# Kernel tuning notes

Measured on AMD Instinct MI355X. Metric: run time of the kernel, lower is better.

The kernel has to match this reference:

```python
import jax, jax.numpy as jnp
import numpy as np

D, NH, NKV, HD, DFF, W, PLD = 2048, 8, 2, 256, 8192, 512, 256
EPS = 1e-6

def rmsnorm(x, w):
    # Gemma-style RMSNorm with (1 + weight) scaling
    return x * jax.lax.rsqrt(jnp.mean(x * x, axis=-1, keepdims=True) + EPS) * (1.0 + w)

def rmsnorm_nw(x):
    # v_norm: weightless RMSNorm
    return x * jax.lax.rsqrt(jnp.mean(x * x, axis=-1, keepdims=True) + EPS)

def rotate_half(x):
    x1, x2 = jnp.split(x, 2, axis=-1)
    return jnp.concatenate([-x2, x1], axis=-1)

def setup_inputs() -> dict:
    key = jax.random.key(0)
    ks = jax.random.split(key, 24)
    w = lambda k, shp, s=0.02: (jax.random.normal(k, shp, dtype=jnp.float32) * s)
    inp = {
        "hidden_states": jax.random.normal(ks[0], (1, 1, D), dtype=jnp.float32),
        "cos": jax.random.uniform(ks[1], (1, 1, HD), dtype=jnp.float32),
        "sin": jax.random.uniform(ks[2], (1, 1, HD), dtype=jnp.float32),
        "mask": jnp.zeros((1, 1, 1, W), dtype=jnp.float32),
        "kv_cache": jnp.zeros((2, NKV, W, HD), dtype=jnp.float32),
        "per_layer": jax.random.normal(ks[3], (1, 1, PLD), dtype=jnp.float32),
        "ln_in_w": w(ks[4], (D,)),
        "Wq": w(ks[5], (NH * HD, D)),
        "q_norm_w": w(ks[6], (HD,)),
        "Wk": w(ks[7], (NKV * HD, D)),
        "Wv": w(ks[8], (NKV * HD, D)),
        "k_norm_w": w(ks[9], (HD,)),
        "Wo": w(ks[10], (D, NH * HD)),
        "post_attn_ln_w": w(ks[11], (D,)),
        "pre_ffn_ln_w": w(ks[12], (D,)),
        "Wgate": w(ks[13], (DFF, D)),
        "Wup": w(ks[14], (DFF, D)),
        "Wdown": w(ks[15], (D, DFF)),
        "post_ffn_ln_w": w(ks[16], (D,)),
        "Wpl_gate": w(ks[17], (PLD, D)),
        "Wpl_proj": w(ks[18], (D, PLD)),
        "post_pl_ln_w": w(ks[19], (D,)),
        "layer_scalar": jnp.ones((1,), dtype=jnp.float32),
        "ring_pos": 37,
    }
    return inp

def reference(hidden_states, cos, sin, mask, kv_cache, per_layer,
              ln_in_w, Wq, q_norm_w, Wk, Wv, k_norm_w, Wo,
              post_attn_ln_w, pre_ffn_ln_w, Wgate, Wup, Wdown, post_ffn_ln_w,
              Wpl_gate, Wpl_proj, post_pl_ln_w, layer_scalar, ring_pos):
    n_rep = NH // NKV
    x = hidden_states[0, 0]                      # (D,)
    residual = x
    h = rmsnorm(x, ln_in_w)                      # input_layernorm
    c, s = cos[0, 0], sin[0, 0]                  # (HD,)
    # q/k/v projections (seq=1 decode -> GEMV)
    q = (h @ Wq.T).reshape(NH, HD)
    q = rmsnorm(q, q_norm_w)
    q = q * c + rotate_half(q) * s               # RoPE
    k = (h @ Wk.T).reshape(NKV, HD)
    k = rmsnorm(k, k_norm_w)
    k = k * c + rotate_half(k) * s
    v = rmsnorm_nw((h @ Wv.T).reshape(NKV, HD))
    # slice-write into the ring-buffer KV cache
    kv = kv_cache.at[0, :, ring_pos, :].set(k).at[1, :, ring_pos, :].set(v)
    K, V = kv[0], kv[1]                          # (NKV, W, HD)
    # GQA: repeat kv heads n_rep times
    Kx = jnp.repeat(K, n_rep, axis=0)            # (NH, W, HD)
    Vx = jnp.repeat(V, n_rep, axis=0)
    scores = jnp.einsum('hd,hwd->hw', q, Kx) + mask[0, 0, 0]   # no 1/sqrt(hd), as in source
    attn = jax.nn.softmax(scores, axis=-1)
    o = jnp.einsum('hw,hwd->hd', attn, Vx).reshape(NH * HD)
    attn_out = rmsnorm(o @ Wo.T, post_attn_ln_w)
    x = residual + attn_out
    # gated-GELU MLP
    residual = x
    hn = rmsnorm(x, pre_ffn_ln_w)
    gate = jax.nn.gelu(hn @ Wgate.T, approximate=True)
    mlp = ((gate * (hn @ Wup.T)) @ Wdown.T)
    x = residual + rmsnorm(mlp, post_ffn_ln_w)
    # per-layer input gate/projection
    residual = x
    g = jax.nn.gelu(x @ Wpl_gate.T, approximate=True) * per_layer[0, 0]
    g = rmsnorm(g @ Wpl_proj.T, post_pl_ln_w)
    x = (residual + g) * layer_scalar[0]
    return x.reshape(1, 1, D)

if __name__ == '__main__':
    out = reference(**setup_inputs())
    print(out.shape, out.dtype)
```

## Files before the change

kernel.cpp:

```cpp
#include <hip/hip_runtime.h>
#include <math.h>

#define D 2048
#define NH 8
#define NKV 2
#define HD 256
#define DFF 8192
#define W 512
#define PLD 256
#define EPS 1e-6f

typedef float f32x4 __attribute__((ext_vector_type(4)));

__device__ __forceinline__ f32x4 ntld(const float* p) {
    return __builtin_nontemporal_load(reinterpret_cast<const f32x4*>(p));
}
__device__ __forceinline__ f32x4 ld4(const float* p) {
    return *reinterpret_cast<const f32x4*>(p);
}
__device__ __forceinline__ float dot4(f32x4 a, f32x4 b, float acc) {
    return fmaf(a.x, b.x, fmaf(a.y, b.y, fmaf(a.z, b.z, fmaf(a.w, b.w, acc))));
}

__device__ __forceinline__ float wave_sum(float v) {
    #pragma unroll
    for (int off = 32; off > 0; off >>= 1) v += __shfl_xor(v, off, 64);
    return v;
}
__device__ __forceinline__ float wave_max(float v) {
    #pragma unroll
    for (int off = 32; off > 0; off >>= 1) v = fmaxf(v, __shfl_xor(v, off, 64));
    return v;
}

__device__ __forceinline__ float gelu_tanh(float x) {
    const float c = 0.7978845608028654f;
    float t = tanhf(c * (x + 0.044715f * x * x * x));
    return 0.5f * x * (1.0f + t);
}

__global__ __launch_bounds__(256, 1)
void qkv_fused(const float* __restrict__ Wq, const float* __restrict__ Wk,
               const float* __restrict__ Wv, const float* __restrict__ x,
               const float* __restrict__ lnw, float* __restrict__ qraw,
               float* __restrict__ kraw, float* __restrict__ vraw) {
    int lane = threadIdx.x & 63, wid = threadIdx.x >> 6;
    int row = blockIdx.x * 4 + wid;
    const float* wr;
    float* outp;
    if (row < 2048)      { wr = Wq + (size_t)row * D;          outp = qraw + row; }
    else if (row < 2560) { wr = Wk + (size_t)(row - 2048) * D; outp = kraw + (row - 2048); }
    else                 { wr = Wv + (size_t)(row - 2560) * D; outp = vraw + (row - 2560); }
    f32x4 xv[8], lw[8];
    #pragma unroll
    for (int c = 0; c < 8; c++) xv[c] = ld4(x + c * 256 + lane * 4);
    #pragma unroll
    for (int c = 0; c < 8; c++) lw[c] = ld4(lnw + c * 256 + lane * 4);
    f32x4 wv4[8];
    #pragma unroll
    for (int c = 0; c < 8; c++) wv4[c] = ntld(wr + c * 256 + lane * 4);
    float ss = 0.f;
    #pragma unroll
    for (int c = 0; c < 8; c++) ss = dot4(xv[c], xv[c], ss);
    ss = wave_sum(ss);
    float rs = rsqrtf(ss / (float)D + EPS);
    float acc = 0.f;
    #pragma unroll
    for (int c = 0; c < 8; c++) {
        f32x4 h4 = xv[c] * rs * (1.f + lw[c]);
        acc = dot4(wv4[c], h4, acc);
    }
    acc = wave_sum(acc);
    if (lane == 0) *outp = acc;
}

__global__ __launch_bounds__(256, 1)
void attn_scores_f(const float* __restrict__ kvc, const float* __restrict__ qraw,
                   const float* __restrict__ kraw, const float* __restrict__ qw,
                   const float* __restrict__ kw, const float* __restrict__ cosv,
                   const float* __restrict__ sinv, const float* __restrict__ mask,
                   const int* __restrict__ ring_p, float* __restrict__ scores) {
    __shared__ float qn[HD], kn[HD];
    int t = threadIdx.x, wv = t >> 6, lane = t & 63;
    int head = blockIdx.x >> 3, wc = blockIdx.x & 7, kvh = head >> 2;
    int ring = *ring_p;
    if (wv == 0) {
        f32x4 v4 = ld4(qraw + head * HD + lane * 4);
        float ss = wave_sum(dot4(v4, v4, 0.f));
        float rs = rsqrtf(ss / (float)HD + EPS);
        f32x4 w4 = ld4(qw + lane * 4);
        f32x4 nv = v4 * rs * (1.f + w4);
        f32x4 pr;
        pr.x = __shfl_xor(nv.x, 32, 64);
        pr.y = __shfl_xor(nv.y, 32, 64);
        pr.z = __shfl_xor(nv.z, 32, 64);
        pr.w = __shfl_xor(nv.w, 32, 64);
        f32x4 c4 = ld4(cosv + lane * 4), s4 = ld4(sinv + lane * 4);
        float sgn = (lane < 32) ? -1.f : 1.f;
        *reinterpret_cast<f32x4*>(qn + lane * 4) = nv * c4 + pr * s4 * sgn;
    } else if (wv == 1) {
        f32x4 v4 = ld4(kraw + kvh * HD + lane * 4);
        float ss = wave_sum(dot4(v4, v4, 0.f));
        float rs = rsqrtf(ss / (float)HD + EPS);
        f32x4 w4 = ld4(kw + lane * 4);
        f32x4 nv = v4 * rs * (1.f + w4);
        f32x4 pr;
        pr.x = __shfl_xor(nv.x, 32, 64);
        pr.y = __shfl_xor(nv.y, 32, 64);
        pr.z = __shfl_xor(nv.z, 32, 64);
        pr.w = __shfl_xor(nv.w, 32, 64);
        f32x4 c4 = ld4(cosv + lane * 4), s4 = ld4(sinv + lane * 4);
        float sgn = (lane < 32) ? -1.f : 1.f;
        *reinterpret_cast<f32x4*>(kn + lane * 4) = nv * c4 + pr * s4 * sgn;
    }
    __syncthreads();
    f32x4 qq = *reinterpret_cast<f32x4*>(qn + lane * 4);
    f32x4 krg = *reinterpret_cast<f32x4*>(kn + lane * 4);
    const float* Kb = kvc + (size_t)kvh * W * HD;
    #pragma unroll 4
    for (int i = 0; i < 16; i++) {
        int w = wc * 64 + wv * 16 + i;
        f32x4 k4 = (w == ring) ? krg : ld4(Kb + (size_t)w * HD + lane * 4);
        float s = wave_sum(dot4(qq, k4, 0.f));
        if (lane == 0) scores[head * W + w] = s + mask[w];
    }
}

__global__ __launch_bounds__(256, 1)
void attn_softmax(float* __restrict__ scores, float* __restrict__ attn_o) {
    __shared__ float s4[4];
    int head = blockIdx.x, t = threadIdx.x, lane = t & 63, wv = t >> 6;
    float s0 = scores[head * W + t], s1 = scores[head * W + 256 + t];
    float m = wave_max(fmaxf(s0, s1));
    if (lane == 0) s4[wv] = m;
    __syncthreads();
    m = fmaxf(fmaxf(s4[0], s4[1]), fmaxf(s4[2], s4[3]));
    __syncthreads();
    float e0 = expf(s0 - m), e1 = expf(s1 - m);
    float se = wave_sum(e0 + e1);
    if (lane == 0) s4[wv] = se;
    __syncthreads();
    float tot = s4[0] + s4[1] + s4[2] + s4[3];
    float inv = 1.f / tot;
    scores[head * W + t] = e0 * inv;
    scores[head * W + 256 + t] = e1 * inv;
    attn_o[head * HD + t] = 0.f;
}

__global__ __launch_bounds__(256, 1)
void attn_pv(const float* __restrict__ kvc, const float* __restrict__ vraw,
             const float* __restrict__ p, const int* __restrict__ ring_p,
             float* __restrict__ attn_o) {
    int t = threadIdx.x, lane = t & 63;
    int head = blockIdx.x >> 3, wc = blockIdx.x & 7, kvh = head >> 2;
    int ring = *ring_p;
    f32x4 v4 = ld4(vraw + kvh * HD + lane * 4);
    float ss = wave_sum(dot4(v4, v4, 0.f));
    float rs = rsqrtf(ss / (float)HD + EPS);
    float vr = vraw[kvh * HD + t] * rs;
    const float* Vb = kvc + (size_t)(NKV + kvh) * W * HD;
    float acc = 0.f;
    #pragma unroll 8
    for (int i = 0; i < 64; i++) {
        int w = wc * 64 + i;
        float vv = (w == ring) ? vr : Vb[(size_t)w * HD + t];
        acc = fmaf(p[head * W + w], vv, acc);
    }
    atomicAdd(&attn_o[head * HD + t], acc);
}

__global__ __launch_bounds__(256, 1)
void gemv2048_nt(const float* __restrict__ Wm, const float* __restrict__ x,
                 float* __restrict__ y) {
    int lane = threadIdx.x & 63, wid = threadIdx.x >> 6;
    int row = blockIdx.x * 4 + wid;
    const float* wr = Wm + (size_t)row * D;
    f32x4 xv[8], w[8];
    #pragma unroll
    for (int c = 0; c < 8; c++) xv[c] = ld4(x + c * 256 + lane * 4);
    #pragma unroll
    for (int c = 0; c < 8; c++) w[c] = ntld(wr + c * 256 + lane * 4);
    float acc = 0.f;
    #pragma unroll
    for (int c = 0; c < 8; c++) acc = dot4(w[c], xv[c], acc);
    acc = wave_sum(acc);
    if (lane == 0) y[row] = acc;
}

__global__ __launch_bounds__(256, 1)
void gateup_fused(const float* __restrict__ Wg, const float* __restrict__ Wu,
                  const float* __restrict__ x, const float* __restrict__ ywo,
                  const float* __restrict__ w_pa, const float* __restrict__ w_pf,
                  float* __restrict__ act, float* __restrict__ x1out) {
    int lane = threadIdx.x & 63, wid = threadIdx.x >> 6;
    int row = blockIdx.x * 4 + wid;
    const float* wg = Wg + (size_t)row * D;
    const float* wu = Wu + (size_t)row * D;
    f32x4 y4[8], xr4[8], w1[8], w2[8];
    #pragma unroll
    for (int c = 0; c < 8; c++) y4[c] = ld4(ywo + c * 256 + lane * 4);
    #pragma unroll
    for (int c = 0; c < 8; c++) xr4[c] = ld4(x + c * 256 + lane * 4);
    #pragma unroll
    for (int c = 0; c < 8; c++) w1[c] = ld4(w_pa + c * 256 + lane * 4);
    #pragma unroll
    for (int c = 0; c < 8; c++) w2[c] = ld4(w_pf + c * 256 + lane * 4);
    f32x4 g4[8], u4[8];
    #pragma unroll
    for (int c = 0; c < 8; c++) g4[c] = ntld(wg + c * 256 + lane * 4);
    #pragma unroll
    for (int c = 0; c < 8; c++) u4[c] = ntld(wu + c * 256 + lane * 4);
    float ss = 0.f;
    #pragma unroll
    for (int c = 0; c < 8; c++) ss = dot4(y4[c], y4[c], ss);
    ss = wave_sum(ss);
    float rs1 = rsqrtf(ss / (float)D + EPS);
    f32x4 x1v[8];
    float s2 = 0.f;
    #pragma unroll
    for (int c = 0; c < 8; c++) {
        f32x4 v = xr4[c] + y4[c] * rs1 * (1.f + w1[c]);
        x1v[c] = v;
        s2 = dot4(v, v, s2);
    }
    s2 = wave_sum(s2);
    float rs2 = rsqrtf(s2 / (float)D + EPS);
    if (blockIdx.x == 0 && wid == 0) {
        #pragma unroll
        for (int c = 0; c < 8; c++)
            *reinterpret_cast<f32x4*>(x1out + c * 256 + lane * 4) = x1v[c];
    }
    float ag = 0.f, au = 0.f;
    #pragma unroll
    for (int c = 0; c < 8; c++) {
        f32x4 h4 = x1v[c] * rs2 * (1.f + w2[c]);
        ag = dot4(g4[c], h4, ag);
        au = dot4(u4[c], h4, au);
    }
    ag = wave_sum(ag);
    au = wave_sum(au);
    if (lane == 0) act[row] = gelu_tanh(ag) * au;
}

__global__ __launch_bounds__(256, 1)
void down_nt(const float* __restrict__ Wd, const float* __restrict__ act,
             float* __restrict__ y) {
    int lane = threadIdx.x & 63, wid = threadIdx.x >> 6;
    int row = blockIdx.x * 4 + wid;
    const float* wr = Wd + (size_t)row * DFF;
    f32x4 wA[8], wB[8], a[8];
    float acc = 0.f;
    #pragma unroll
    for (int c = 0; c < 8; c++) a[c] = ld4(act + c * 256 + lane * 4);
    #pragma unroll
    for (int c = 0; c < 8; c++) wA[c] = ntld(wr + c * 256 + lane * 4);
    #pragma unroll
    for (int c = 0; c < 8; c++) wB[c] = ntld(wr + 2048 + c * 256 + lane * 4);
    #pragma unroll
    for (int c = 0; c < 8; c++) acc = dot4(wA[c], a[c], acc);
    #pragma unroll
    for (int c = 0; c < 8; c++) a[c] = ld4(act + 2048 + c * 256 + lane * 4);
    #pragma unroll
    for (int c = 0; c < 8; c++) wA[c] = ntld(wr + 4096 + c * 256 + lane * 4);
    #pragma unroll
    for (int c = 0; c < 8; c++) acc = dot4(wB[c], a[c], acc);
    #pragma unroll
    for (int c = 0; c < 8; c++) a[c] = ld4(act + 4096 + c * 256 + lane * 4);
    #pragma unroll
    for (int c = 0; c < 8; c++) wB[c] = ntld(wr + 6144 + c * 256 + lane * 4);
    #pragma unroll
    for (int c = 0; c < 8; c++) acc = dot4(wA[c], a[c], acc);
    #pragma unroll
    for (int c = 0; c < 8; c++) a[c] = ld4(act + 6144 + c * 256 + lane * 4);
    #pragma unroll
    for (int c = 0; c < 8; c++) acc = dot4(wB[c], a[c], acc);
    acc = wave_sum(acc);
    if (lane == 0) y[row] = acc;
}

__global__ __launch_bounds__(256, 1)
void plgate_fused(const float* __restrict__ Wpl, const float* __restrict__ x1,
                  const float* __restrict__ y2, const float* __restrict__ w_pf,
                  const float* __restrict__ per_layer, float* __restrict__ g,
                  float* __restrict__ x2out) {
    int lane = threadIdx.x & 63, wid = threadIdx.x >> 6;
    int row = blockIdx.x * 4 + wid;
    f32x4 y4[8], x4[8], w4[8];
    #pragma unroll
    for (int c = 0; c < 8; c++) y4[c] = ld4(y2 + c * 256 + lane * 4);
    #pragma unroll
    for (int c = 0; c < 8; c++) x4[c] = ld4(x1 + c * 256 + lane * 4);
    #pragma unroll
    for (int c = 0; c < 8; c++) w4[c] = ld4(w_pf + c * 256 + lane * 4);
    f32x4 wv4[8];
    const float* wr = Wpl + (size_t)row * D;
    #pragma unroll
    for (int c = 0; c < 8; c++) wv4[c] = ntld(wr + c * 256 + lane * 4);
    float ss = 0.f;
    #pragma unroll
    for (int c = 0; c < 8; c++) ss = dot4(y4[c], y4[c], ss);
    ss = wave_sum(ss);
    float rs = rsqrtf(ss / (float)D + EPS);
    f32x4 x2v[8];
    #pragma unroll
    for (int c = 0; c < 8; c++) x2v[c] = x4[c] + y4[c] * rs * (1.f + w4[c]);
    if (blockIdx.x == 0 && wid == 0) {
        #pragma unroll
        for (int c = 0; c < 8; c++)
            *reinterpret_cast<f32x4*>(x2out + c * 256 + lane * 4) = x2v[c];
    }
    float acc = 0.f;
    #pragma unroll
    for (int c = 0; c < 8; c++) acc = dot4(wv4[c], x2v[c], acc);
    acc = wave_sum(acc);
    if (lane == 0) g[row] = gelu_tanh(acc) * per_layer[row];
}

__global__ __launch_bounds__(256, 1)
void gemv256_nt(const float* __restrict__ Wm, const float* __restrict__ x,
                float* __restrict__ y) {
    int lane = threadIdx.x & 63, wid = threadIdx.x >> 6;
    int row = blockIdx.x * 4 + wid;
    f32x4 x0 = ld4(x + lane * 4);
    f32x4 w0 = ntld(Wm + (size_t)row * PLD + lane * 4);
    float acc = dot4(w0, x0, 0.f);
    acc = wave_sum(acc);
    if (lane == 0) y[row] = acc;
}

__global__ __launch_bounds__(256, 1)
void final_fused(const float* __restrict__ x2, const float* __restrict__ g2,
                 const float* __restrict__ w, const float* __restrict__ scal,
                 float* __restrict__ out) {
    int lane = threadIdx.x & 63;
    f32x4 g4[8];
    #pragma unroll
    for (int c = 0; c < 8; c++) g4[c] = ld4(g2 + c * 256 + lane * 4);
    float ss = 0.f;
    #pragma unroll
    for (int c = 0; c < 8; c++) ss = dot4(g4[c], g4[c], ss);
    ss = wave_sum(ss);
    float rs = rsqrtf(ss / (float)D + EPS);
    int idx = blockIdx.x * 256 + threadIdx.x;
    out[idx] = (x2[idx] + g2[idx] * rs * (1.f + w[idx])) * scal[0];
}

extern "C" void kernel_launch(void* const* d_in, const int* in_sizes, int n_in,
                              void* d_out, int out_size, void* d_ws, size_t ws_size,
                              hipStream_t stream) {
    const float* x_in        = (const float*)d_in[0];
    const float* cosv        = (const float*)d_in[1];
    const float* sinv        = (const float*)d_in[2];
    const float* mask        = (const float*)d_in[3];
    const float* kvc         = (const float*)d_in[4];
    const float* per_layer   = (const float*)d_in[5];
    const float* ln_in_w     = (const float*)d_in[6];
    const float* Wq          = (const float*)d_in[7];
    const float* q_norm_w    = (const float*)d_in[8];
    const float* Wk          = (const float*)d_in[9];
    const float* Wv          = (const float*)d_in[10];
    const float* k_norm_w    = (const float*)d_in[11];
    const float* Wo          = (const float*)d_in[12];
    const float* post_attn_w = (const float*)d_in[13];
    const float* pre_ffn_w   = (const float*)d_in[14];
    const float* Wgate       = (const float*)d_in[15];
    const float* Wup         = (const float*)d_in[16];
    const float* Wdown       = (const float*)d_in[17];
    const float* post_ffn_w  = (const float*)d_in[18];
    const float* Wpl_gate    = (const float*)d_in[19];
    const float* Wpl_proj    = (const float*)d_in[20];
    const float* post_pl_w   = (const float*)d_in[21];
    const float* layer_scal  = (const float*)d_in[22];
    const int*   ring_pos    = (const int*)d_in[23];
    float* out = (float*)d_out;
    float* ws  = (float*)d_ws;

    float* qraw   = ws;
    float* kraw   = ws + 2048;
    float* vraw   = ws + 2560;
    float* scores = ws + 3072;
    float* attn_o = ws + 7168;
    float* y_wo   = ws + 9216;
    float* x1     = ws + 11264;
    float* act    = ws + 13312;
    float* y2     = ws + 21504;
    float* x2     = ws + 23552;
    float* g      = ws + 25600;
    float* g2     = ws + 25856;

    qkv_fused<<<768, 256, 0, stream>>>(Wq, Wk, Wv, x_in, ln_in_w, qraw, kraw, vraw);
    attn_scores_f<<<64, 256, 0, stream>>>(kvc, qraw, kraw, q_norm_w, k_norm_w,
                                          cosv, sinv, mask, ring_pos, scores);
    attn_softmax<<<8, 256, 0, stream>>>(scores, attn_o);
    attn_pv<<<64, 256, 0, stream>>>(kvc, vraw, scores, ring_pos, attn_o);
    gemv2048_nt<<<512, 256, 0, stream>>>(Wo, attn_o, y_wo);
    gateup_fused<<<2048, 256, 0, stream>>>(Wgate, Wup, x_in, y_wo,
                                           post_attn_w, pre_ffn_w, act, x1);
    down_nt<<<512, 256, 0, stream>>>(Wdown, act, y2);
    plgate_fused<<<64, 256, 0, stream>>>(Wpl_gate, x1, y2, post_ffn_w,
                                         per_layer, g, x2);
    gemv256_nt<<<512, 256, 0, stream>>>(Wpl_proj, g, g2);
    final_fused<<<8, 256, 0, stream>>>(x2, g2, post_pl_w, layer_scal, out);
}
```

Baseline: 74.71 us.

## Fuse softmax into PV kernel and reduce PV partials inside Wo GEMV

Removes the separate softmax launch by having each PV block recompute the head's softmax into shared memory. It replaces the atomicAdd accumulation with per-chunk partial outputs that the Wo GEMV sums on load. It also reorders the QKV and gate/up kernels to compute the normalized input before issuing weight loads, which cuts live registers. The cost is redundant softmax work across 8 blocks per head and 8x more partial reads in every Wo block.

```diff
diff --git a/kernel.cpp b/kernel.cpp
--- a/kernel.cpp
+++ b/kernel.cpp
@@ -56,20 +56,20 @@
     for (int c = 0; c < 8; c++) xv[c] = ld4(x + c * 256 + lane * 4);
     #pragma unroll
     for (int c = 0; c < 8; c++) lw[c] = ld4(lnw + c * 256 + lane * 4);
-    f32x4 wv4[8];
-    #pragma unroll
-    for (int c = 0; c < 8; c++) wv4[c] = ntld(wr + c * 256 + lane * 4);
     float ss = 0.f;
     #pragma unroll
     for (int c = 0; c < 8; c++) ss = dot4(xv[c], xv[c], ss);
     ss = wave_sum(ss);
     float rs = rsqrtf(ss / (float)D + EPS);
+    f32x4 h[8];
+    #pragma unroll
+    for (int c = 0; c < 8; c++) h[c] = xv[c] * rs * (1.f + lw[c]);
+    f32x4 wv4[8];
+    #pragma unroll
+    for (int c = 0; c < 8; c++) wv4[c] = ntld(wr + c * 256 + lane * 4);
     float acc = 0.f;
     #pragma unroll
-    for (int c = 0; c < 8; c++) {
-        f32x4 h4 = xv[c] * rs * (1.f + lw[c]);
-        acc = dot4(wv4[c], h4, acc);
-    }
+    for (int c = 0; c < 8; c++) acc = dot4(wv4[c], h[c], acc);
     acc = wave_sum(acc);
     if (lane == 0) *outp = acc;
 }
@@ -127,9 +127,14 @@
 }
 
 __global__ __launch_bounds__(256, 1)
-void attn_softmax(float* __restrict__ scores, float* __restrict__ attn_o) {
+void attn_pv_part(const float* __restrict__ kvc, const float* __restrict__ vraw,
+                  const float* __restrict__ scores, const int* __restrict__ ring_p,
+                  float* __restrict__ part) {
     __shared__ float s4[4];
-    int head = blockIdx.x, t = threadIdx.x, lane = t & 63, wv = t >> 6;
+    __shared__ float pch[W];
+    int t = threadIdx.x, lane = t & 63, wv = t >> 6;
+    int head = blockIdx.x >> 3, wc = blockIdx.x & 7, kvh = head >> 2;
+    int ring = *ring_p;
     float s0 = scores[head * W + t], s1 = scores[head * W + 256 + t];
     float m = wave_max(fmaxf(s0, s1));
     if (lane == 0) s4[wv] = m;
@@ -140,46 +145,43 @@
     float se = wave_sum(e0 + e1);
     if (lane == 0) s4[wv] = se;
     __syncthreads();
-    float tot = s4[0] + s4[1] + s4[2] + s4[3];
-    float inv = 1.f / tot;
-    scores[head * W + t] = e0 * inv;
-    scores[head * W + 256 + t] = e1 * inv;
-    attn_o[head * HD + t] = 0.f;
-}
-
-__global__ __launch_bounds__(256, 1)
-void attn_pv(const float* __restrict__ kvc, const float* __restrict__ vraw,
-             const float* __restrict__ p, const int* __restrict__ ring_p,
-             float* __restrict__ attn_o) {
-    int t = threadIdx.x, lane = t & 63;
-    int head = blockIdx.x >> 3, wc = blockIdx.x & 7, kvh = head >> 2;
-    int ring = *ring_p;
+    float inv = 1.f / (s4[0] + s4[1] + s4[2] + s4[3]);
+    pch[t] = e0 * inv;
+    pch[t + 256] = e1 * inv;
     f32x4 v4 = ld4(vraw + kvh * HD + lane * 4);
-    float ss = wave_sum(dot4(v4, v4, 0.f));
-    float rs = rsqrtf(ss / (float)HD + EPS);
-    float vr = vraw[kvh * HD + t] * rs;
+    float ssv = wave_sum(dot4(v4, v4, 0.f));
+    float rsv = rsqrtf(ssv / (float)HD + EPS);
+    float vr = vraw[kvh * HD + t] * rsv;
+    __syncthreads();
     const float* Vb = kvc + (size_t)(NKV + kvh) * W * HD;
     float acc = 0.f;
     #pragma unroll 8
     for (int i = 0; i < 64; i++) {
         int w = wc * 64 + i;
         float vv = (w == ring) ? vr : Vb[(size_t)w * HD + t];
-        acc = fmaf(p[head * W + w], vv, acc);
-    }
-    atomicAdd(&attn_o[head * HD + t], acc);
-}
-
-__global__ __launch_bounds__(256, 1)
-void gemv2048_nt(const float* __restrict__ Wm, const float* __restrict__ x,
-                 float* __restrict__ y) {
+        acc = fmaf(pch[w], vv, acc);
+    }
+    part[(size_t)(head * 8 + wc) * 256 + t] = acc;
+}
+
+__global__ __launch_bounds__(256, 1)
+void wo_fused(const float* __restrict__ Wm, const float* __restrict__ part,
+              float* __restrict__ y) {
     int lane = threadIdx.x & 63, wid = threadIdx.x >> 6;
     int row = blockIdx.x * 4 + wid;
     const float* wr = Wm + (size_t)row * D;
-    f32x4 xv[8], w[8];
-    #pragma unroll
-    for (int c = 0; c < 8; c++) xv[c] = ld4(x + c * 256 + lane * 4);
+    f32x4 w[8];
     #pragma unroll
     for (int c = 0; c < 8; c++) w[c] = ntld(wr + c * 256 + lane * 4);
+    f32x4 xv[8];
+    #pragma unroll
+    for (int c = 0; c < 8; c++) {
+        f32x4 s = ld4(part + (size_t)(c * 8) * 256 + lane * 4);
+        #pragma unroll
+        for (int wc = 1; wc < 8; wc++)
+            s += ld4(part + (size_t)(c * 8 + wc) * 256 + lane * 4);
+        xv[c] = s;
+    }
     float acc = 0.f;
     #pragma unroll
     for (int c = 0; c < 8; c++) acc = dot4(w[c], xv[c], acc);
@@ -196,47 +198,44 @@
     int row = blockIdx.x * 4 + wid;
     const float* wg = Wg + (size_t)row * D;
     const float* wu = Wu + (size_t)row * D;
-    f32x4 y4[8], xr4[8], w1[8], w2[8];
-    #pragma unroll
-    for (int c = 0; c < 8; c++) y4[c] = ld4(ywo + c * 256 + lane * 4);
-    #pragma unroll
-    for (int c = 0; c < 8; c++) xr4[c] = ld4(x + c * 256 + lane * 4);
-    #pragma unroll
-    for (int c = 0; c < 8; c++) w1[c] = ld4(w_pa + c * 256 + lane * 4);
-    #pragma unroll
-    for (int c = 0; c < 8; c++) w2[c] = ld4(w_pf + c * 256 + lane * 4);
-    f32x4 g4[8], u4[8];
-    #pragma unroll
-    for (int c = 0; c < 8; c++) g4[c] = ntld(wg + c * 256 + lane * 4);
-    #pragma unroll
-    for (int c = 0; c < 8; c++) u4[c] = ntld(wu + c * 256 + lane * 4);
+    f32x4 x1v[8];
     float ss = 0.f;
-    #pragma unroll
-    for (int c = 0; c < 8; c++) ss = dot4(y4[c], y4[c], ss);
-    ss = wave_sum(ss);
-    float rs1 = rsqrtf(ss / (float)D + EPS);
-    f32x4 x1v[8];
-    float s2 = 0.f;
-    #pragma unroll
-    for (int c = 0; c < 8; c++) {
-        f32x4 v = xr4[c] + y4[c] * rs1 * (1.f + w1[c]);
-        x1v[c] = v;
-        s2 = dot4(v, v, s2);
-    }
-    s2 = wave_sum(s2);
-    float rs2 = rsqrtf(s2 / (float)D + EPS);
+    {
+        f32x4 y4[8];
+        #pragma unroll
+        for (int c = 0; c < 8; c++) y4[c] = ld4(ywo + c * 256 + lane * 4);
+        #pragma unroll
+        for (int c = 0; c < 8; c++) ss = dot4(y4[c], y4[c], ss);
+        ss = wave_sum(ss);
+        float rs1 = rsqrtf(ss / (float)D + EPS);
+        float s2 = 0.f;
+        #pragma unroll
+        for (int c = 0; c < 8; c++) {
+            f32x4 v = ld4(x + c * 256 + lane * 4)
+                    + y4[c] * rs1 * (1.f + ld4(w_pa + c * 256 + lane * 4));
+            x1v[c] = v;
+            s2 = dot4(v, v, s2);
+        }
+        ss = wave_sum(s2);
+    }
+    float rs2 = rsqrtf(ss / (float)D + EPS);
     if (blockIdx.x == 0 && wid == 0) {
         #pragma unroll
         for (int c = 0; c < 8; c++)
             *reinterpret_cast<f32x4*>(x1out + c * 256 + lane * 4) = x1v[c];
     }
+    f32x4 h[8];
+    #pragma unroll
+    for (int c = 0; c < 8; c++)
+        h[c] = x1v[c] * rs2 * (1.f + ld4(w_pf + c * 256 + lane * 4));
+    f32x4 g4[8], u4[8];
+    #pragma unroll
+    for (int c = 0; c < 8; c++) g4[c] = ntld(wg + c * 256 + lane * 4);
+    #pragma unroll
+    for (int c = 0; c < 8; c++) u4[c] = ntld(wu + c * 256 + lane * 4);
     float ag = 0.f, au = 0.f;
     #pragma unroll
-    for (int c = 0; c < 8; c++) {
-        f32x4 h4 = x1v[c] * rs2 * (1.f + w2[c]);
-        ag = dot4(g4[c], h4, ag);
-        au = dot4(u4[c], h4, au);
-    }
+    for (int c = 0; c < 8; c++) { ag = dot4(g4[c], h[c], ag); au = dot4(u4[c], h[c], au); }
     ag = wave_sum(ag);
     au = wave_sum(au);
     if (lane == 0) act[row] = gelu_tanh(ag) * au;
@@ -379,21 +378,20 @@
     float* kraw   = ws + 2048;
     float* vraw   = ws + 2560;
     float* scores = ws + 3072;
-    float* attn_o = ws + 7168;
-    float* y_wo   = ws + 9216;
-    float* x1     = ws + 11264;
-    float* act    = ws + 13312;
-    float* y2     = ws + 21504;
-    float* x2     = ws + 23552;
-    float* g      = ws + 25600;
-    float* g2     = ws + 25856;
+    float* part   = ws + 7168;
+    float* y_wo   = ws + 23552;
+    float* x1     = ws + 25600;
+    float* act    = ws + 27648;
+    float* y2     = ws + 35840;
+    float* x2     = ws + 37888;
+    float* g      = ws + 39936;
+    float* g2     = ws + 40192;
 
     qkv_fused<<<768, 256, 0, stream>>>(Wq, Wk, Wv, x_in, ln_in_w, qraw, kraw, vraw);
     attn_scores_f<<<64, 256, 0, stream>>>(kvc, qraw, kraw, q_norm_w, k_norm_w,
                                           cosv, sinv, mask, ring_pos, scores);
-    attn_softmax<<<8, 256, 0, stream>>>(scores, attn_o);
-    attn_pv<<<64, 256, 0, stream>>>(kvc, vraw, scores, ring_pos, attn_o);
-    gemv2048_nt<<<512, 256, 0, stream>>>(Wo, attn_o, y_wo);
+    attn_pv_part<<<64, 256, 0, stream>>>(kvc, vraw, scores, ring_pos, part);
+    wo_fused<<<512, 256, 0, stream>>>(Wo, part, y_wo);
     gateup_fused<<<2048, 256, 0, stream>>>(Wgate, Wup, x_in, y_wo,
                                            post_attn_w, pre_ffn_w, act, x1);
     down_nt<<<512, 256, 0, stream>>>(Wdown, act, y2);
```

Measured after the change: 77.78 us. 1.04x slower.
